# Kernel tuning notes

Measured on AMD Instinct MI355X. Metric: run time of the kernel, lower is better.

Reference implementation:

```python
import jax, jax.numpy as jnp
import numpy as np

N_NODES = 50000
N_EDGES = 800000
D = 128  # in_dim == hidden_dim


def setup_inputs() -> dict:
    key = jax.random.key(0)
    k1, k2, k3, k4 = jax.random.split(key, 4)
    x = jax.random.normal(k1, (N_NODES, D), dtype=jnp.float32)
    edge_index = jax.random.randint(k2, (2, N_EDGES), 0, N_NODES, dtype=jnp.int64)
    # Glorot-ish scale for square weights
    scale = 1.0 / np.sqrt(D)
    W1 = jax.random.normal(k3, (D, D), dtype=jnp.float32) * scale
    W2 = jax.random.normal(k4, (D, D), dtype=jnp.float32) * scale
    b1 = jnp.zeros((D,), dtype=jnp.float32)
    b2 = jnp.zeros((D,), dtype=jnp.float32)
    return {"x": x, "edge_index": edge_index, "W1": W1, "b1": b1, "W2": W2, "b2": b2}


def _gcn_layer(x, W, b, src, dst, norm, n):
    # PyG GCNConv: h = x @ W, then symmetric-normalized scatter-add, then + bias
    h = x @ W                                   # [N, D] dense GEMM
    msg = h[src] * norm[:, None]                # [E', D] gather + scale
    out = jax.ops.segment_sum(msg, dst, num_segments=n)  # scatter-add
    return out + b


def reference(x, edge_index, W1, b1, W2, b2):
    n = x.shape[0]
    # add self-loops (GCNConv default add_self_loops=True)
    loops = jnp.arange(n, dtype=edge_index.dtype)
    src = jnp.concatenate([edge_index[0], loops])
    dst = jnp.concatenate([edge_index[1], loops])
    # symmetric normalization: deg^{-1/2}[src] * deg^{-1/2}[dst]
    deg = jax.ops.segment_sum(jnp.ones_like(src, dtype=x.dtype), dst, num_segments=n)
    dinv = jax.lax.rsqrt(jnp.maximum(deg, 1.0))  # deg >= 1 due to self-loops
    norm = dinv[src] * dinv[dst]
    # layer 1: conv -> relu (dropout is identity in eval mode)
    h = jax.nn.relu(_gcn_layer(x, W1, b1, src, dst, norm, n))
    # layer 2 (cut='c2'): conv -> relu
    h = jax.nn.relu(_gcn_layer(h, W2, b2, src, dst, norm, n))
    return h
```

## Files before the change

### kernel.cpp

```cpp
#include <hip/hip_runtime.h>

#define NN 50000
#define NE 800000
#define DD 128
#define NSTRIP 3125
#define NB 196
#define CHUNK 4096
#define MAXB 6144

#define OF_LCNT  0
#define OF_LOFS  50176
#define OF_DINV  100352
#define OF_OFFS2 150528
#define OF_TMP2  250624
#define OF_CSRU  1053440
#define OF_H1    1655552
#define OF_H2    4855552
#define OF_W1H   8055552
#define OF_W1L   8063744
#define OF_W2H   8071936
#define OF_W2L   8080128

typedef __attribute__((ext_vector_type(8))) short bf8_t;
typedef __attribute__((ext_vector_type(8))) unsigned short us8;
typedef __attribute__((ext_vector_type(4))) float f32x4;

static __device__ __forceinline__ unsigned short f2bf(float f) {
    unsigned int u = __float_as_uint(f);
    unsigned int r = (u + 0x7fffu + ((u >> 16) & 1u)) >> 16;
    return (unsigned short)r;
}
static __device__ __forceinline__ float bf2f(unsigned short h) {
    return __uint_as_float(((unsigned int)h) << 16);
}

__global__ void k_wconv(const float* __restrict__ W1, const float* __restrict__ W2,
                        ushort* __restrict__ w1h, ushort* __restrict__ w1l,
                        ushort* __restrict__ w2h, ushort* __restrict__ w2l) {
    int gg = blockIdx.x * 256 + threadIdx.x;
    const float* W = (gg < 2048) ? W1 : W2;
    ushort* wh = (gg < 2048) ? w1h : w2h;
    ushort* wl = (gg < 2048) ? w1l : w2l;
    int g = gg & 2047;
    int ntile = g >> 8;
    int kk = (g >> 6) & 3;
    int lane = g & 63;
    int k0 = kk * 32 + ((lane >> 4) * 8);
    int col = ntile * 16 + (lane & 15);
#pragma unroll
    for (int j = 0; j < 8; ++j) {
        float w = W[(k0 + j) * DD + col];
        unsigned short h = f2bf(w);
        wh[(size_t)g * 8 + j] = h;
        wl[(size_t)g * 8 + j] = f2bf(w - bf2f(h));
    }
}

__global__ __launch_bounds__(256) void k_prep(
        const int* __restrict__ src, const int* __restrict__ dst,
        int* __restrict__ lcnt_g, int* __restrict__ lofs_g,
        unsigned int* __restrict__ tmp2,
        const float* __restrict__ X,
        const ushort* __restrict__ wh, const ushort* __restrict__ wl,
        ushort* __restrict__ H1) {
    __shared__ int lcnt[256];
    __shared__ int lsc[256];
    __shared__ int lcur[256];
    int tid = threadIdx.x;
    if (blockIdx.x < 196) {
        int blk = blockIdx.x;
        lcnt[tid] = 0;
        __syncthreads();
        int e0 = blk * CHUNK;
        int e1 = e0 + CHUNK; if (e1 > NE) e1 = NE;
        for (int e = e0 + tid; e < e1; e += 256)
            atomicAdd(&lcnt[dst[e] >> 8], 1);
        __syncthreads();
        int v = lcnt[tid];
        lsc[tid] = v;
        __syncthreads();
        for (int o = 1; o < 256; o <<= 1) {
            int t = (tid >= o) ? lsc[tid - o] : 0;
            __syncthreads();
            lsc[tid] += t;
            __syncthreads();
        }
        int excl = lsc[tid] - v;
        lcnt_g[tid * 196 + blk] = v;
        lofs_g[tid * 196 + blk] = excl;
        lcur[tid] = excl;
        __syncthreads();
        for (int e = e0 + tid; e < e1; e += 256) {
            int d = dst[e], s = src[e];
            int b = d >> 8;
            int r = atomicAdd(&lcur[b], 1);
            tmp2[blk * CHUNK + r] = ((unsigned int)s << 8) | (unsigned int)(d & 255);
        }
        return;
    }
    int wave = tid >> 6;
    int lane = tid & 63;
    int strip = (blockIdx.x - 196) * 4 + wave;
    if (strip >= NSTRIP) return;
    int rb = strip << 4;
    int m = lane & 15;
    int quad = lane >> 4;
    const float* ar = X + (size_t)(rb + m) * DD;
    f32x4 acc[8];
#pragma unroll
    for (int t = 0; t < 8; ++t) acc[t] = (f32x4){0.f, 0.f, 0.f, 0.f};
#pragma unroll
    for (int kk = 0; kk < 4; ++kk) {
        float4 xa = *(const float4*)(ar + kk * 32 + quad * 8);
        float4 xb = *(const float4*)(ar + kk * 32 + quad * 8 + 4);
        float xs[8] = {xa.x, xa.y, xa.z, xa.w, xb.x, xb.y, xb.z, xb.w};
        bf8_t ah, al;
#pragma unroll
        for (int j = 0; j < 8; ++j) {
            unsigned short hh = f2bf(xs[j]);
            ah[j] = (short)hh;
            al[j] = (short)f2bf(xs[j] - bf2f(hh));
        }
#pragma unroll
        for (int t = 0; t < 8; ++t) {
            size_t bo = ((size_t)(t * 4 + kk) * 64 + lane) * 8;
            bf8_t bh = *(const bf8_t*)(wh + bo);
            bf8_t bl = *(const bf8_t*)(wl + bo);
            acc[t] = __builtin_amdgcn_mfma_f32_16x16x32_bf16(ah, bh, acc[t], 0, 0, 0);
            acc[t] = __builtin_amdgcn_mfma_f32_16x16x32_bf16(ah, bl, acc[t], 0, 0, 0);
            acc[t] = __builtin_amdgcn_mfma_f32_16x16x32_bf16(al, bh, acc[t], 0, 0, 0);
        }
    }
#pragma unroll
    for (int t = 0; t < 8; ++t) {
#pragma unroll
        for (int r = 0; r < 4; ++r)
            H1[(size_t)(rb + quad * 4 + r) * DD + t * 16 + m] = f2bf(acc[t][r]);
    }
}

__global__ __launch_bounds__(256) void k_sort(const int* __restrict__ lcnt_g,
                                              const int* __restrict__ lofs_g,
                                              const unsigned int* __restrict__ tmp2,
                                              ushort* __restrict__ csru,
                                              int2* __restrict__ offs2,
                                              float* __restrict__ dinv) {
    __shared__ unsigned int ent[MAXB];
    __shared__ int c[256];
    __shared__ int p[256];
    __shared__ int o[256];
    __shared__ int cnt[256];
    __shared__ int boff[256];
    __shared__ int cur[256];
    int b = blockIdx.x, tid = threadIdx.x;
    int cv = (tid < 196) ? lcnt_g[b * 196 + tid] : 0;
    o[tid] = (tid < 196) ? lofs_g[b * 196 + tid] : 0;
    c[tid] = cv;
    p[tid] = cv;
    cnt[tid] = 0;
    __syncthreads();
    for (int s = 1; s < 256; s <<= 1) {
        int t = (tid >= s) ? p[tid - s] : 0;
        __syncthreads();
        p[tid] += t;
        __syncthreads();
    }
    int nb = p[255];
    for (int i = tid; i < nb; i += 256) {
        int lo = 0, hi = 255;
#pragma unroll
        for (int it = 0; it < 8; ++it) {
            int mid = (lo + hi) >> 1;
            if (p[mid] > i) hi = mid; else lo = mid + 1;
        }
        int blk = lo;
        int j = i - (p[blk] - c[blk]);
        unsigned int e = tmp2[blk * CHUNK + o[blk] + j];
        ent[i] = e;
        atomicAdd(&cnt[e & 255], 1);
    }
    __syncthreads();
    int v = cnt[tid];
    boff[tid] = v;
    __syncthreads();
    for (int s = 1; s < 256; s <<= 1) {
        int t = (tid >= s) ? boff[tid - s] : 0;
        __syncthreads();
        boff[tid] += t;
        __syncthreads();
    }
    int excl = boff[tid] - v;
    int base = b * MAXB;
    int node = b * 256 + tid;
    if (node < NN) {
        offs2[node] = make_int2(base + excl, base + excl + v);
        dinv[node] = rsqrtf((float)(v + 1));
    }
    cur[tid] = excl;
    __syncthreads();
    for (int i = tid; i < nb; i += 256) {
        unsigned int e = ent[i];
        int bin = e & 255;
        int r = atomicAdd(&cur[bin], 1);
        csru[base + r] = (ushort)(e >> 8);
    }
}

__global__ __launch_bounds__(512) void k_aggmm(const ushort* __restrict__ h1,
                                               const float* __restrict__ dinv,
                                               const int2* __restrict__ offs2,
                                               const ushort* __restrict__ csru,
                                               const float* __restrict__ b1,
                                               const ushort* __restrict__ w2h,
                                               const ushort* __restrict__ w2l,
                                               ushort* __restrict__ h2) {
    __shared__ float xs[16][136];
    int wave = threadIdx.x >> 6;
    int lane = threadIdx.x & 63;
    int rb = blockIdx.x * 16;
    int q = lane >> 4;
    int l = lane & 15;
    const float* bp = b1 + 8 * l;
    for (int nn = 0; nn < 2; ++nn) {
        int node = rb + wave * 2 + nn;
        float a0[8] = {0.f, 0.f, 0.f, 0.f, 0.f, 0.f, 0.f, 0.f};
        float a1[8] = {0.f, 0.f, 0.f, 0.f, 0.f, 0.f, 0.f, 0.f};
        float a2[8] = {0.f, 0.f, 0.f, 0.f, 0.f, 0.f, 0.f, 0.f};
        float a3[8] = {0.f, 0.f, 0.f, 0.f, 0.f, 0.f, 0.f, 0.f};
        int2 oe = offs2[node];
        int e  = oe.x + q;
        int e1 = oe.y;
        for (; e + 12 < e1; e += 16) {
            int s0 = csru[e];
            int s1 = csru[e + 4];
            int s2 = csru[e + 8];
            int s3 = csru[e + 12];
            float w0 = dinv[s0], w1 = dinv[s1], w2 = dinv[s2], w3 = dinv[s3];
            us8 v0 = *(const us8*)(h1 + (size_t)s0 * DD + 8 * l);
            us8 v1 = *(const us8*)(h1 + (size_t)s1 * DD + 8 * l);
            us8 v2 = *(const us8*)(h1 + (size_t)s2 * DD + 8 * l);
            us8 v3 = *(const us8*)(h1 + (size_t)s3 * DD + 8 * l);
#pragma unroll
            for (int j = 0; j < 8; ++j) {
                a0[j] += w0 * bf2f(v0[j]);
                a1[j] += w1 * bf2f(v1[j]);
                a2[j] += w2 * bf2f(v2[j]);
                a3[j] += w3 * bf2f(v3[j]);
            }
        }
        for (; e < e1; e += 4) {
            int s0 = csru[e];
            float w0 = dinv[s0];
            us8 v0 = *(const us8*)(h1 + (size_t)s0 * DD + 8 * l);
#pragma unroll
            for (int j = 0; j < 8; ++j) a0[j] += w0 * bf2f(v0[j]);
        }
        float dnode = dinv[node];
        if (q == 0) {
            us8 v = *(const us8*)(h1 + (size_t)node * DD + 8 * l);
#pragma unroll
            for (int j = 0; j < 8; ++j) a0[j] += dnode * bf2f(v[j]);
        }
#pragma unroll
        for (int j = 0; j < 8; ++j) {
            a0[j] += a1[j] + a2[j] + a3[j];
            a0[j] += __shfl_xor(a0[j], 16, 64);
            a0[j] += __shfl_xor(a0[j], 32, 64);
        }
        if (q == 0) {
            float* xr = &xs[wave * 2 + nn][8 * l];
#pragma unroll
            for (int j = 0; j < 8; ++j)
                xr[j] = fmaxf(dnode * a0[j] + bp[j], 0.f);
        }
    }
    __syncthreads();
    int m = lane & 15;
    int quad = lane >> 4;
    int t = wave;
    f32x4 acc = (f32x4){0.f, 0.f, 0.f, 0.f};
#pragma unroll
    for (int kk = 0; kk < 4; ++kk) {
        const float* xr = &xs[m][kk * 32 + quad * 8];
        float4 xa = *(const float4*)xr;
        float4 xb = *(const float4*)(xr + 4);
        float xv[8] = {xa.x, xa.y, xa.z, xa.w, xb.x, xb.y, xb.z, xb.w};
        bf8_t ah, al;
#pragma unroll
        for (int j = 0; j < 8; ++j) {
            unsigned short hh = f2bf(xv[j]);
            ah[j] = (short)hh;
            al[j] = (short)f2bf(xv[j] - bf2f(hh));
        }
        size_t bo = ((size_t)(t * 4 + kk) * 64 + lane) * 8;
        bf8_t bh = *(const bf8_t*)(w2h + bo);
        bf8_t bl = *(const bf8_t*)(w2l + bo);
        acc = __builtin_amdgcn_mfma_f32_16x16x32_bf16(ah, bh, acc, 0, 0, 0);
        acc = __builtin_amdgcn_mfma_f32_16x16x32_bf16(ah, bl, acc, 0, 0, 0);
        acc = __builtin_amdgcn_mfma_f32_16x16x32_bf16(al, bh, acc, 0, 0, 0);
    }
#pragma unroll
    for (int r = 0; r < 4; ++r)
        h2[(size_t)(rb + quad * 4 + r) * DD + t * 16 + m] = f2bf(acc[r]);
}

__global__ void k_agg(const ushort* __restrict__ h, const float* __restrict__ dinv,
                      const int2* __restrict__ offs2, const ushort* __restrict__ csru,
                      const float* __restrict__ bias, float* __restrict__ outf) {
    int wave = threadIdx.x >> 6;
    int lane = threadIdx.x & 63;
    int node = blockIdx.x * 4 + wave;
    int q = lane >> 4;
    int l = lane & 15;
    float a0[8] = {0.f, 0.f, 0.f, 0.f, 0.f, 0.f, 0.f, 0.f};
    float a1[8] = {0.f, 0.f, 0.f, 0.f, 0.f, 0.f, 0.f, 0.f};
    float a2[8] = {0.f, 0.f, 0.f, 0.f, 0.f, 0.f, 0.f, 0.f};
    float a3[8] = {0.f, 0.f, 0.f, 0.f, 0.f, 0.f, 0.f, 0.f};
    int2 oe = offs2[node];
    int e  = oe.x + q;
    int e1 = oe.y;
    for (; e + 12 < e1; e += 16) {
        int s0 = csru[e];
        int s1 = csru[e + 4];
        int s2 = csru[e + 8];
        int s3 = csru[e + 12];
        float w0 = dinv[s0], w1 = dinv[s1], w2 = dinv[s2], w3 = dinv[s3];
        us8 v0 = *(const us8*)(h + (size_t)s0 * DD + 8 * l);
        us8 v1 = *(const us8*)(h + (size_t)s1 * DD + 8 * l);
        us8 v2 = *(const us8*)(h + (size_t)s2 * DD + 8 * l);
        us8 v3 = *(const us8*)(h + (size_t)s3 * DD + 8 * l);
#pragma unroll
        for (int j = 0; j < 8; ++j) {
            a0[j] += w0 * bf2f(v0[j]);
            a1[j] += w1 * bf2f(v1[j]);
            a2[j] += w2 * bf2f(v2[j]);
            a3[j] += w3 * bf2f(v3[j]);
        }
    }
    for (; e < e1; e += 4) {
        int s0 = csru[e];
        float w0 = dinv[s0];
        us8 v0 = *(const us8*)(h + (size_t)s0 * DD + 8 * l);
#pragma unroll
        for (int j = 0; j < 8; ++j) a0[j] += w0 * bf2f(v0[j]);
    }
    float dnode = dinv[node];
    if (q == 0) {
        us8 v = *(const us8*)(h + (size_t)node * DD + 8 * l);
#pragma unroll
        for (int j = 0; j < 8; ++j) a0[j] += dnode * bf2f(v[j]);
    }
#pragma unroll
    for (int j = 0; j < 8; ++j) {
        a0[j] += a1[j] + a2[j] + a3[j];
        a0[j] += __shfl_xor(a0[j], 16, 64);
        a0[j] += __shfl_xor(a0[j], 32, 64);
    }
    if (q == 0) {
        float* op = outf + (size_t)node * DD + 8 * l;
        const float* bp = bias + 8 * l;
        float4 o0, o1;
        o0.x = fmaxf(dnode * a0[0] + bp[0], 0.f);
        o0.y = fmaxf(dnode * a0[1] + bp[1], 0.f);
        o0.z = fmaxf(dnode * a0[2] + bp[2], 0.f);
        o0.w = fmaxf(dnode * a0[3] + bp[3], 0.f);
        o1.x = fmaxf(dnode * a0[4] + bp[4], 0.f);
        o1.y = fmaxf(dnode * a0[5] + bp[5], 0.f);
        o1.z = fmaxf(dnode * a0[6] + bp[6], 0.f);
        o1.w = fmaxf(dnode * a0[7] + bp[7], 0.f);
        *(float4*)op = o0;
        *(float4*)(op + 4) = o1;
    }
}

extern "C" void kernel_launch(void* const* d_in, const int* in_sizes, int n_in,
                              void* d_out, int out_size, void* d_ws, size_t ws_size,
                              hipStream_t stream) {
    const float* x  = (const float*)d_in[0];
    const int*   ei = (const int*)d_in[1];
    const float* W1 = (const float*)d_in[2];
    const float* b1 = (const float*)d_in[3];
    const float* W2 = (const float*)d_in[4];
    const float* b2 = (const float*)d_in[5];
    float* out = (float*)d_out;

    const int* src = ei;
    const int* dst = ei + NE;

    int*          wsi  = (int*)d_ws;
    float*        wsf  = (float*)d_ws;
    ushort*       wsu  = (ushort*)d_ws;
    unsigned int* wsuw = (unsigned int*)d_ws;
    int*    lcnt_g = wsi + OF_LCNT;
    int*    lofs_g = wsi + OF_LOFS;
    float*  dinv   = wsf + OF_DINV;
    int2*   offs2  = (int2*)(wsi + OF_OFFS2);
    unsigned int* tmp2 = wsuw + OF_TMP2;
    ushort* csru   = wsu + (size_t)OF_CSRU * 2;
    ushort* h1     = wsu + (size_t)OF_H1 * 2;
    ushort* h2     = wsu + (size_t)OF_H2 * 2;
    ushort* w1h    = wsu + (size_t)OF_W1H * 2;
    ushort* w1l    = wsu + (size_t)OF_W1L * 2;
    ushort* w2h    = wsu + (size_t)OF_W2H * 2;
    ushort* w2l    = wsu + (size_t)OF_W2L * 2;

    hipLaunchKernelGGL(k_wconv, dim3(16), dim3(256), 0, stream,
                       W1, W2, w1h, w1l, w2h, w2l);
    hipLaunchKernelGGL(k_prep, dim3(196 + (NSTRIP + 3) / 4), dim3(256), 0, stream,
                       src, dst, lcnt_g, lofs_g, tmp2, x, w1h, w1l, h1);
    hipLaunchKernelGGL(k_sort, dim3(NB), dim3(256), 0, stream,
                       lcnt_g, lofs_g, tmp2, csru, offs2, dinv);
    hipLaunchKernelGGL(k_aggmm, dim3(NSTRIP), dim3(512), 0, stream,
                       h1, dinv, offs2, csru, b1, w2h, w2l, h2);
    hipLaunchKernelGGL(k_agg, dim3(NN / 4), dim3(256), 0, stream,
                       h2, dinv, offs2, csru, b2, out);
}
```

Before: 208.0 us.

## Prescale features by source dinv and split fused aggregate-GEMM into separate kernels

Source-side normalization is folded into the features ahead of time. k_sort writes g1 = dinv*h1, and the layer-2 GEMM writes g2 = dinv*(x@W2), so the aggregation loops drop the per-edge dinv gather and multiply. The fused k_aggmm kernel is replaced by a templated k_agg that writes hi/lo bf16 splits, followed by a standalone MFMA GEMM kernel. This removes random dinv loads per edge but adds a launch, extra hi/lo intermediate traffic through global memory, and an extra bf16 rounding of the prescaled features.

```diff
diff --git a/kernel.cpp b/kernel.cpp
--- a/kernel.cpp
+++ b/kernel.cpp
@@ -15,11 +15,14 @@
 #define OF_TMP2  250624
 #define OF_CSRU  1053440
 #define OF_H1    1655552
-#define OF_H2    4855552
-#define OF_W1H   8055552
-#define OF_W1L   8063744
-#define OF_W2H   8071936
-#define OF_W2L   8080128
+#define OF_G1    4855552
+#define OF_XH    8055552
+#define OF_XL    11255552
+#define OF_G2    14455552
+#define OF_W1H   17655552
+#define OF_W1L   17663744
+#define OF_W2H   17671936
+#define OF_W2L   17680128
 
 typedef __attribute__((ext_vector_type(8))) short bf8_t;
 typedef __attribute__((ext_vector_type(8))) unsigned short us8;
@@ -144,7 +147,9 @@
                                               const unsigned int* __restrict__ tmp2,
                                               ushort* __restrict__ csru,
                                               int2* __restrict__ offs2,
-                                              float* __restrict__ dinv) {
+                                              float* __restrict__ dinv,
+                                              const ushort* __restrict__ h1,
+                                              ushort* __restrict__ g1) {
     __shared__ unsigned int ent[MAXB];
     __shared__ int c[256];
     __shared__ int p[256];
@@ -152,6 +157,7 @@
     __shared__ int cnt[256];
     __shared__ int boff[256];
     __shared__ int cur[256];
+    __shared__ float sdinv[256];
     int b = blockIdx.x, tid = threadIdx.x;
     int cv = (tid < 196) ? lcnt_g[b * 196 + tid] : 0;
     o[tid] = (tid < 196) ? lofs_g[b * 196 + tid] : 0;
@@ -192,9 +198,11 @@
     int excl = boff[tid] - v;
     int base = b * MAXB;
     int node = b * 256 + tid;
+    float dv = rsqrtf((float)(v + 1));
+    sdinv[tid] = dv;
     if (node < NN) {
         offs2[node] = make_int2(base + excl, base + excl + v);
-        dinv[node] = rsqrtf((float)(v + 1));
+        dinv[node] = dv;
     }
     cur[tid] = excl;
     __syncthreads();
@@ -204,109 +212,26 @@
         int r = atomicAdd(&cur[bin], 1);
         csru[base + r] = (ushort)(e >> 8);
     }
-}
-
-__global__ __launch_bounds__(512) void k_aggmm(const ushort* __restrict__ h1,
-                                               const float* __restrict__ dinv,
-                                               const int2* __restrict__ offs2,
-                                               const ushort* __restrict__ csru,
-                                               const float* __restrict__ b1,
-                                               const ushort* __restrict__ w2h,
-                                               const ushort* __restrict__ w2l,
-                                               ushort* __restrict__ h2) {
-    __shared__ float xs[16][136];
-    int wave = threadIdx.x >> 6;
-    int lane = threadIdx.x & 63;
-    int rb = blockIdx.x * 16;
-    int q = lane >> 4;
-    int l = lane & 15;
-    const float* bp = b1 + 8 * l;
-    for (int nn = 0; nn < 2; ++nn) {
-        int node = rb + wave * 2 + nn;
-        float a0[8] = {0.f, 0.f, 0.f, 0.f, 0.f, 0.f, 0.f, 0.f};
-        float a1[8] = {0.f, 0.f, 0.f, 0.f, 0.f, 0.f, 0.f, 0.f};
-        float a2[8] = {0.f, 0.f, 0.f, 0.f, 0.f, 0.f, 0.f, 0.f};
-        float a3[8] = {0.f, 0.f, 0.f, 0.f, 0.f, 0.f, 0.f, 0.f};
-        int2 oe = offs2[node];
-        int e  = oe.x + q;
-        int e1 = oe.y;
-        for (; e + 12 < e1; e += 16) {
-            int s0 = csru[e];
-            int s1 = csru[e + 4];
-            int s2 = csru[e + 8];
-            int s3 = csru[e + 12];
-            float w0 = dinv[s0], w1 = dinv[s1], w2 = dinv[s2], w3 = dinv[s3];
-            us8 v0 = *(const us8*)(h1 + (size_t)s0 * DD + 8 * l);
-            us8 v1 = *(const us8*)(h1 + (size_t)s1 * DD + 8 * l);
-            us8 v2 = *(const us8*)(h1 + (size_t)s2 * DD + 8 * l);
-            us8 v3 = *(const us8*)(h1 + (size_t)s3 * DD + 8 * l);
-#pragma unroll
-            for (int j = 0; j < 8; ++j) {
-                a0[j] += w0 * bf2f(v0[j]);
-                a1[j] += w1 * bf2f(v1[j]);
-                a2[j] += w2 * bf2f(v2[j]);
-                a3[j] += w3 * bf2f(v3[j]);
-            }
-        }
-        for (; e < e1; e += 4) {
-            int s0 = csru[e];
-            float w0 = dinv[s0];
-            us8 v0 = *(const us8*)(h1 + (size_t)s0 * DD + 8 * l);
-#pragma unroll
-            for (int j = 0; j < 8; ++j) a0[j] += w0 * bf2f(v0[j]);
-        }
-        float dnode = dinv[node];
-        if (q == 0) {
-            us8 v = *(const us8*)(h1 + (size_t)node * DD + 8 * l);
-#pragma unroll
-            for (int j = 0; j < 8; ++j) a0[j] += dnode * bf2f(v[j]);
-        }
-#pragma unroll
-        for (int j = 0; j < 8; ++j) {
-            a0[j] += a1[j] + a2[j] + a3[j];
-            a0[j] += __shfl_xor(a0[j], 16, 64);
-            a0[j] += __shfl_xor(a0[j], 32, 64);
-        }
-        if (q == 0) {
-            float* xr = &xs[wave * 2 + nn][8 * l];
-#pragma unroll
-            for (int j = 0; j < 8; ++j)
-                xr[j] = fmaxf(dnode * a0[j] + bp[j], 0.f);
-        }
-    }
-    __syncthreads();
-    int m = lane & 15;
-    int quad = lane >> 4;
-    int t = wave;
-    f32x4 acc = (f32x4){0.f, 0.f, 0.f, 0.f};
-#pragma unroll
-    for (int kk = 0; kk < 4; ++kk) {
-        const float* xr = &xs[m][kk * 32 + quad * 8];
-        float4 xa = *(const float4*)xr;
-        float4 xb = *(const float4*)(xr + 4);
-        float xv[8] = {xa.x, xa.y, xa.z, xa.w, xb.x, xb.y, xb.z, xb.w};
-        bf8_t ah, al;
-#pragma unroll
-        for (int j = 0; j < 8; ++j) {
-            unsigned short hh = f2bf(xv[j]);
-            ah[j] = (short)hh;
-            al[j] = (short)f2bf(xv[j] - bf2f(hh));
-        }
-        size_t bo = ((size_t)(t * 4 + kk) * 64 + lane) * 8;
-        bf8_t bh = *(const bf8_t*)(w2h + bo);
-        bf8_t bl = *(const bf8_t*)(w2l + bo);
-        acc = __builtin_amdgcn_mfma_f32_16x16x32_bf16(ah, bh, acc, 0, 0, 0);
-        acc = __builtin_amdgcn_mfma_f32_16x16x32_bf16(ah, bl, acc, 0, 0, 0);
-        acc = __builtin_amdgcn_mfma_f32_16x16x32_bf16(al, bh, acc, 0, 0, 0);
-    }
-#pragma unroll
-    for (int r = 0; r < 4; ++r)
-        h2[(size_t)(rb + quad * 4 + r) * DD + t * 16 + m] = f2bf(acc[r]);
-}
-
-__global__ void k_agg(const ushort* __restrict__ h, const float* __restrict__ dinv,
+    int rmax = NN - b * 256;
+    if (rmax > 256) rmax = 256;
+    for (int ci = tid; ci < rmax * 16; ci += 256) {
+        int row = ci >> 4;
+        int c8 = ci & 15;
+        float dd = sdinv[row];
+        size_t idx = ((size_t)(b * 256 + row)) * DD + c8 * 8;
+        us8 hv = *(const us8*)(h1 + idx);
+        us8 gv;
+#pragma unroll
+        for (int j = 0; j < 8; ++j) gv[j] = f2bf(dd * bf2f(hv[j]));
+        *(us8*)(g1 + idx) = gv;
+    }
+}
+
+template <int OUTMODE>
+__global__ void k_agg(const ushort* __restrict__ g, const float* __restrict__ dinv,
                       const int2* __restrict__ offs2, const ushort* __restrict__ csru,
-                      const float* __restrict__ bias, float* __restrict__ outf) {
+                      const float* __restrict__ bias, float* __restrict__ outf,
+                      ushort* __restrict__ oh, ushort* __restrict__ ol) {
     int wave = threadIdx.x >> 6;
     int lane = threadIdx.x & 63;
     int node = blockIdx.x * 4 + wave;
@@ -324,31 +249,28 @@
         int s1 = csru[e + 4];
         int s2 = csru[e + 8];
         int s3 = csru[e + 12];
-        float w0 = dinv[s0], w1 = dinv[s1], w2 = dinv[s2], w3 = dinv[s3];
-        us8 v0 = *(const us8*)(h + (size_t)s0 * DD + 8 * l);
-        us8 v1 = *(const us8*)(h + (size_t)s1 * DD + 8 * l);
-        us8 v2 = *(const us8*)(h + (size_t)s2 * DD + 8 * l);
-        us8 v3 = *(const us8*)(h + (size_t)s3 * DD + 8 * l);
+        us8 v0 = *(const us8*)(g + (size_t)s0 * DD + 8 * l);
+        us8 v1 = *(const us8*)(g + (size_t)s1 * DD + 8 * l);
+        us8 v2 = *(const us8*)(g + (size_t)s2 * DD + 8 * l);
+        us8 v3 = *(const us8*)(g + (size_t)s3 * DD + 8 * l);
 #pragma unroll
         for (int j = 0; j < 8; ++j) {
-            a0[j] += w0 * bf2f(v0[j]);
-            a1[j] += w1 * bf2f(v1[j]);
-            a2[j] += w2 * bf2f(v2[j]);
-            a3[j] += w3 * bf2f(v3[j]);
+            a0[j] += bf2f(v0[j]);
+            a1[j] += bf2f(v1[j]);
+            a2[j] += bf2f(v2[j]);
+            a3[j] += bf2f(v3[j]);
         }
     }
     for (; e < e1; e += 4) {
         int s0 = csru[e];
-        float w0 = dinv[s0];
-        us8 v0 = *(const us8*)(h + (size_t)s0 * DD + 8 * l);
-#pragma unroll
-        for (int j = 0; j < 8; ++j) a0[j] += w0 * bf2f(v0[j]);
-    }
-    float dnode = dinv[node];
+        us8 v0 = *(const us8*)(g + (size_t)s0 * DD + 8 * l);
+#pragma unroll
+        for (int j = 0; j < 8; ++j) a0[j] += bf2f(v0[j]);
+    }
     if (q == 0) {
-        us8 v = *(const us8*)(h + (size_t)node * DD + 8 * l);
-#pragma unroll
-        for (int j = 0; j < 8; ++j) a0[j] += dnode * bf2f(v[j]);
+        us8 v = *(const us8*)(g + (size_t)node * DD + 8 * l);
+#pragma unroll
+        for (int j = 0; j < 8; ++j) a0[j] += bf2f(v[j]);
     }
 #pragma unroll
     for (int j = 0; j < 8; ++j) {
@@ -357,19 +279,71 @@
         a0[j] += __shfl_xor(a0[j], 32, 64);
     }
     if (q == 0) {
-        float* op = outf + (size_t)node * DD + 8 * l;
+        float dnode = dinv[node];
         const float* bp = bias + 8 * l;
-        float4 o0, o1;
-        o0.x = fmaxf(dnode * a0[0] + bp[0], 0.f);
-        o0.y = fmaxf(dnode * a0[1] + bp[1], 0.f);
-        o0.z = fmaxf(dnode * a0[2] + bp[2], 0.f);
-        o0.w = fmaxf(dnode * a0[3] + bp[3], 0.f);
-        o1.x = fmaxf(dnode * a0[4] + bp[4], 0.f);
-        o1.y = fmaxf(dnode * a0[5] + bp[5], 0.f);
-        o1.z = fmaxf(dnode * a0[6] + bp[6], 0.f);
-        o1.w = fmaxf(dnode * a0[7] + bp[7], 0.f);
-        *(float4*)op = o0;
-        *(float4*)(op + 4) = o1;
+        float r[8];
+#pragma unroll
+        for (int j = 0; j < 8; ++j) r[j] = fmaxf(dnode * a0[j] + bp[j], 0.f);
+        if (OUTMODE == 0) {
+            float* op = outf + (size_t)node * DD + 8 * l;
+            float4 o0 = {r[0], r[1], r[2], r[3]};
+            float4 o1 = {r[4], r[5], r[6], r[7]};
+            *(float4*)op = o0;
+            *(float4*)(op + 4) = o1;
+        } else {
+            us8 hh, ll;
+#pragma unroll
+            for (int j = 0; j < 8; ++j) {
+                unsigned short h = f2bf(r[j]);
+                hh[j] = h;
+                ll[j] = f2bf(r[j] - bf2f(h));
+            }
+            *(us8*)(oh + (size_t)node * DD + 8 * l) = hh;
+            *(us8*)(ol + (size_t)node * DD + 8 * l) = ll;
+        }
+    }
+}
+
+__global__ __launch_bounds__(256) void k_mgemm2(const ushort* __restrict__ xh,
+                                                const ushort* __restrict__ xl,
+                                                const ushort* __restrict__ wh,
+                                                const ushort* __restrict__ wl,
+                                                const float* __restrict__ dinv,
+                                                ushort* __restrict__ G) {
+    int wave = threadIdx.x >> 6;
+    int lane = threadIdx.x & 63;
+    int strip = blockIdx.x * 4 + wave;
+    if (strip >= NSTRIP) return;
+    int rb = strip << 4;
+    int m = lane & 15;
+    int quad = lane >> 4;
+    const ushort* arh = xh + (size_t)(rb + m) * DD;
+    const ushort* arl = xl + (size_t)(rb + m) * DD;
+    f32x4 acc[8];
+#pragma unroll
+    for (int t = 0; t < 8; ++t) acc[t] = (f32x4){0.f, 0.f, 0.f, 0.f};
+#pragma unroll
+    for (int kk = 0; kk < 4; ++kk) {
+        bf8_t ah = *(const bf8_t*)(arh + kk * 32 + quad * 8);
+        bf8_t al = *(const bf8_t*)(arl + kk * 32 + quad * 8);
+#pragma unroll
+        for (int t = 0; t < 8; ++t) {
+            size_t bo = ((size_t)(t * 4 + kk) * 64 + lane) * 8;
+            bf8_t bh = *(const bf8_t*)(wh + bo);
+            bf8_t bl = *(const bf8_t*)(wl + bo);
+            acc[t] = __builtin_amdgcn_mfma_f32_16x16x32_bf16(ah, bh, acc[t], 0, 0, 0);
+            acc[t] = __builtin_amdgcn_mfma_f32_16x16x32_bf16(ah, bl, acc[t], 0, 0, 0);
+            acc[t] = __builtin_amdgcn_mfma_f32_16x16x32_bf16(al, bh, acc[t], 0, 0, 0);
+        }
+    }
+    float dv[4];
+#pragma unroll
+    for (int r = 0; r < 4; ++r) dv[r] = dinv[rb + quad * 4 + r];
+#pragma unroll
+    for (int t = 0; t < 8; ++t) {
+#pragma unroll
+        for (int r = 0; r < 4; ++r)
+            G[(size_t)(rb + quad * 4 + r) * DD + t * 16 + m] = f2bf(dv[r] * acc[t][r]);
     }
 }
 
@@ -398,7 +372,10 @@
     unsigned int* tmp2 = wsuw + OF_TMP2;
     ushort* csru   = wsu + (size_t)OF_CSRU * 2;
     ushort* h1     = wsu + (size_t)OF_H1 * 2;
-    ushort* h2     = wsu + (size_t)OF_H2 * 2;
+    ushort* g1     = wsu + (size_t)OF_G1 * 2;
+    ushort* xh     = wsu + (size_t)OF_XH * 2;
+    ushort* xl     = wsu + (size_t)OF_XL * 2;
+    ushort* g2     = wsu + (size_t)OF_G2 * 2;
     ushort* w1h    = wsu + (size_t)OF_W1H * 2;
     ushort* w1l    = wsu + (size_t)OF_W1L * 2;
     ushort* w2h    = wsu + (size_t)OF_W2H * 2;
@@ -409,9 +386,11 @@
     hipLaunchKernelGGL(k_prep, dim3(196 + (NSTRIP + 3) / 4), dim3(256), 0, stream,
                        src, dst, lcnt_g, lofs_g, tmp2, x, w1h, w1l, h1);
     hipLaunchKernelGGL(k_sort, dim3(NB), dim3(256), 0, stream,
-                       lcnt_g, lofs_g, tmp2, csru, offs2, dinv);
-    hipLaunchKernelGGL(k_aggmm, dim3(NSTRIP), dim3(512), 0, stream,
-                       h1, dinv, offs2, csru, b1, w2h, w2l, h2);
-    hipLaunchKernelGGL(k_agg, dim3(NN / 4), dim3(256), 0, stream,
-                       h2, dinv, offs2, csru, b2, out);
-}
+                       lcnt_g, lofs_g, tmp2, csru, offs2, dinv, h1, g1);
+    hipLaunchKernelGGL(k_agg<1>, dim3(NN / 4), dim3(256), 0, stream,
+                       g1, dinv, offs2, csru, b1, (float*)nullptr, xh, xl);
+    hipLaunchKernelGGL(k_mgemm2, dim3((NSTRIP + 3) / 4), dim3(256), 0, stream,
+                       xh, xl, w2h, w2l, dinv, g2);
+    hipLaunchKernelGGL(k_agg<0>, dim3(NN / 4), dim3(256), 0, stream,
+                       g2, dinv, offs2, csru, b2, out, (ushort*)nullptr, (ushort*)nullptr);
+}
```

Measured after the change: 222.0 us. +6.7%, slower.

## Prescale features by source dinv to remove per-edge dinv gathers

Applied to the files above, without the earlier changes.

Folds the source-side dinv factor into the node features before aggregation. k_sort writes a scaled copy g1 = dinv*h1, and k_aggmm writes g2 already scaled by dinv. The aggregation loops then sum raw rows without gathering dinv[src] per edge and without a multiply per element. In exchange, k_sort gains an extra full read and write pass over h1, and the pre-scaled values are rounded to bf16 a second time, which slightly changes numerics.

```diff
diff --git a/kernel.cpp b/kernel.cpp
--- a/kernel.cpp
+++ b/kernel.cpp
@@ -15,11 +15,12 @@
 #define OF_TMP2  250624
 #define OF_CSRU  1053440
 #define OF_H1    1655552
-#define OF_H2    4855552
-#define OF_W1H   8055552
-#define OF_W1L   8063744
-#define OF_W2H   8071936
-#define OF_W2L   8080128
+#define OF_G1    4855552
+#define OF_G2    8055552
+#define OF_W1H   11255552
+#define OF_W1L   11263744
+#define OF_W2H   11271936
+#define OF_W2L   11280128
 
 typedef __attribute__((ext_vector_type(8))) short bf8_t;
 typedef __attribute__((ext_vector_type(8))) unsigned short us8;
@@ -144,7 +145,9 @@
                                               const unsigned int* __restrict__ tmp2,
                                               ushort* __restrict__ csru,
                                               int2* __restrict__ offs2,
-                                              float* __restrict__ dinv) {
+                                              float* __restrict__ dinv,
+                                              const ushort* __restrict__ h1,
+                                              ushort* __restrict__ g1) {
     __shared__ unsigned int ent[MAXB];
     __shared__ int c[256];
     __shared__ int p[256];
@@ -152,6 +155,7 @@
     __shared__ int cnt[256];
     __shared__ int boff[256];
     __shared__ int cur[256];
+    __shared__ float sdinv[256];
     int b = blockIdx.x, tid = threadIdx.x;
     int cv = (tid < 196) ? lcnt_g[b * 196 + tid] : 0;
     o[tid] = (tid < 196) ? lofs_g[b * 196 + tid] : 0;
@@ -192,9 +196,11 @@
     int excl = boff[tid] - v;
     int base = b * MAXB;
     int node = b * 256 + tid;
+    float dv = rsqrtf((float)(v + 1));
+    sdinv[tid] = dv;
     if (node < NN) {
         offs2[node] = make_int2(base + excl, base + excl + v);
-        dinv[node] = rsqrtf((float)(v + 1));
+        dinv[node] = dv;
     }
     cur[tid] = excl;
     __syncthreads();
@@ -204,17 +210,30 @@
         int r = atomicAdd(&cur[bin], 1);
         csru[base + r] = (ushort)(e >> 8);
     }
-}
-
-__global__ __launch_bounds__(512) void k_aggmm(const ushort* __restrict__ h1,
+    int rmax = NN - b * 256;
+    if (rmax > 256) rmax = 256;
+    for (int ci = tid; ci < rmax * 16; ci += 256) {
+        int row = ci >> 4;
+        int c8 = ci & 15;
+        float dd = sdinv[row];
+        size_t idx = ((size_t)(b * 256 + row)) * DD + c8 * 8;
+        us8 hv = *(const us8*)(h1 + idx);
+        us8 gv;
+#pragma unroll
+        for (int j = 0; j < 8; ++j) gv[j] = f2bf(dd * bf2f(hv[j]));
+        *(us8*)(g1 + idx) = gv;
+    }
+}
+
+__global__ __launch_bounds__(512) void k_aggmm(const ushort* __restrict__ g1,
                                                const float* __restrict__ dinv,
                                                const int2* __restrict__ offs2,
                                                const ushort* __restrict__ csru,
                                                const float* __restrict__ b1,
                                                const ushort* __restrict__ w2h,
                                                const ushort* __restrict__ w2l,
-                                               ushort* __restrict__ h2) {
-    __shared__ float xs[16][136];
+                                               ushort* __restrict__ g2) {
+    __shared__ float xs[16][132];
     int wave = threadIdx.x >> 6;
     int lane = threadIdx.x & 63;
     int rb = blockIdx.x * 16;
@@ -235,31 +254,28 @@
             int s1 = csru[e + 4];
             int s2 = csru[e + 8];
             int s3 = csru[e + 12];
-            float w0 = dinv[s0], w1 = dinv[s1], w2 = dinv[s2], w3 = dinv[s3];
-            us8 v0 = *(const us8*)(h1 + (size_t)s0 * DD + 8 * l);
-            us8 v1 = *(const us8*)(h1 + (size_t)s1 * DD + 8 * l);
-            us8 v2 = *(const us8*)(h1 + (size_t)s2 * DD + 8 * l);
-            us8 v3 = *(const us8*)(h1 + (size_t)s3 * DD + 8 * l);
+            us8 v0 = *(const us8*)(g1 + (size_t)s0 * DD + 8 * l);
+            us8 v1 = *(const us8*)(g1 + (size_t)s1 * DD + 8 * l);
+            us8 v2 = *(const us8*)(g1 + (size_t)s2 * DD + 8 * l);
+            us8 v3 = *(const us8*)(g1 + (size_t)s3 * DD + 8 * l);
 #pragma unroll
             for (int j = 0; j < 8; ++j) {
-                a0[j] += w0 * bf2f(v0[j]);
-                a1[j] += w1 * bf2f(v1[j]);
-                a2[j] += w2 * bf2f(v2[j]);
-                a3[j] += w3 * bf2f(v3[j]);
+                a0[j] += bf2f(v0[j]);
+                a1[j] += bf2f(v1[j]);
+                a2[j] += bf2f(v2[j]);
+                a3[j] += bf2f(v3[j]);
             }
         }
         for (; e < e1; e += 4) {
             int s0 = csru[e];
-            float w0 = dinv[s0];
-            us8 v0 = *(const us8*)(h1 + (size_t)s0 * DD + 8 * l);
-#pragma unroll
-            for (int j = 0; j < 8; ++j) a0[j] += w0 * bf2f(v0[j]);
-        }
-        float dnode = dinv[node];
+            us8 v0 = *(const us8*)(g1 + (size_t)s0 * DD + 8 * l);
+#pragma unroll
+            for (int j = 0; j < 8; ++j) a0[j] += bf2f(v0[j]);
+        }
         if (q == 0) {
-            us8 v = *(const us8*)(h1 + (size_t)node * DD + 8 * l);
-#pragma unroll
-            for (int j = 0; j < 8; ++j) a0[j] += dnode * bf2f(v[j]);
+            us8 v = *(const us8*)(g1 + (size_t)node * DD + 8 * l);
+#pragma unroll
+            for (int j = 0; j < 8; ++j) a0[j] += bf2f(v[j]);
         }
 #pragma unroll
         for (int j = 0; j < 8; ++j) {
@@ -268,6 +284,7 @@
             a0[j] += __shfl_xor(a0[j], 32, 64);
         }
         if (q == 0) {
+            float dnode = dinv[node];
             float* xr = &xs[wave * 2 + nn][8 * l];
 #pragma unroll
             for (int j = 0; j < 8; ++j)
@@ -299,12 +316,15 @@
         acc = __builtin_amdgcn_mfma_f32_16x16x32_bf16(ah, bl, acc, 0, 0, 0);
         acc = __builtin_amdgcn_mfma_f32_16x16x32_bf16(al, bh, acc, 0, 0, 0);
     }
+    float dv[4];
+#pragma unroll
+    for (int r = 0; r < 4; ++r) dv[r] = dinv[rb + quad * 4 + r];
 #pragma unroll
     for (int r = 0; r < 4; ++r)
-        h2[(size_t)(rb + quad * 4 + r) * DD + t * 16 + m] = f2bf(acc[r]);
-}
-
-__global__ void k_agg(const ushort* __restrict__ h, const float* __restrict__ dinv,
+        g2[(size_t)(rb + quad * 4 + r) * DD + t * 16 + m] = f2bf(dv[r] * acc[r]);
+}
+
+__global__ void k_agg(const ushort* __restrict__ g, const float* __restrict__ dinv,
                       const int2* __restrict__ offs2, const ushort* __restrict__ csru,
                       const float* __restrict__ bias, float* __restrict__ outf) {
     int wave = threadIdx.x >> 6;
@@ -324,31 +344,28 @@
         int s1 = csru[e + 4];
         int s2 = csru[e + 8];
         int s3 = csru[e + 12];
-        float w0 = dinv[s0], w1 = dinv[s1], w2 = dinv[s2], w3 = dinv[s3];
-        us8 v0 = *(const us8*)(h + (size_t)s0 * DD + 8 * l);
-        us8 v1 = *(const us8*)(h + (size_t)s1 * DD + 8 * l);
-        us8 v2 = *(const us8*)(h + (size_t)s2 * DD + 8 * l);
-        us8 v3 = *(const us8*)(h + (size_t)s3 * DD + 8 * l);
+        us8 v0 = *(const us8*)(g + (size_t)s0 * DD + 8 * l);
+        us8 v1 = *(const us8*)(g + (size_t)s1 * DD + 8 * l);
+        us8 v2 = *(const us8*)(g + (size_t)s2 * DD + 8 * l);
+        us8 v3 = *(const us8*)(g + (size_t)s3 * DD + 8 * l);
 #pragma unroll
         for (int j = 0; j < 8; ++j) {
-            a0[j] += w0 * bf2f(v0[j]);
-            a1[j] += w1 * bf2f(v1[j]);
-            a2[j] += w2 * bf2f(v2[j]);
-            a3[j] += w3 * bf2f(v3[j]);
+            a0[j] += bf2f(v0[j]);
+            a1[j] += bf2f(v1[j]);
+            a2[j] += bf2f(v2[j]);
+            a3[j] += bf2f(v3[j]);
         }
     }
     for (; e < e1; e += 4) {
         int s0 = csru[e];
-        float w0 = dinv[s0];
-        us8 v0 = *(const us8*)(h + (size_t)s0 * DD + 8 * l);
-#pragma unroll
-        for (int j = 0; j < 8; ++j) a0[j] += w0 * bf2f(v0[j]);
-    }
-    float dnode = dinv[node];
+        us8 v0 = *(const us8*)(g + (size_t)s0 * DD + 8 * l);
+#pragma unroll
+        for (int j = 0; j < 8; ++j) a0[j] += bf2f(v0[j]);
+    }
     if (q == 0) {
-        us8 v = *(const us8*)(h + (size_t)node * DD + 8 * l);
-#pragma unroll
-        for (int j = 0; j < 8; ++j) a0[j] += dnode * bf2f(v[j]);
+        us8 v = *(const us8*)(g + (size_t)node * DD + 8 * l);
+#pragma unroll
+        for (int j = 0; j < 8; ++j) a0[j] += bf2f(v[j]);
     }
 #pragma unroll
     for (int j = 0; j < 8; ++j) {
@@ -357,6 +374,7 @@
         a0[j] += __shfl_xor(a0[j], 32, 64);
     }
     if (q == 0) {
+        float dnode = dinv[node];
         float* op = outf + (size_t)node * DD + 8 * l;
         const float* bp = bias + 8 * l;
         float4 o0, o1;
@@ -398,7 +416,8 @@
     unsigned int* tmp2 = wsuw + OF_TMP2;
     ushort* csru   = wsu + (size_t)OF_CSRU * 2;
     ushort* h1     = wsu + (size_t)OF_H1 * 2;
-    ushort* h2     = wsu + (size_t)OF_H2 * 2;
+    ushort* g1     = wsu + (size_t)OF_G1 * 2;
+    ushort* g2     = wsu + (size_t)OF_G2 * 2;
     ushort* w1h    = wsu + (size_t)OF_W1H * 2;
     ushort* w1l    = wsu + (size_t)OF_W1L * 2;
     ushort* w2h    = wsu + (size_t)OF_W2H * 2;
@@ -409,9 +428,9 @@
     hipLaunchKernelGGL(k_prep, dim3(196 + (NSTRIP + 3) / 4), dim3(256), 0, stream,
                        src, dst, lcnt_g, lofs_g, tmp2, x, w1h, w1l, h1);
     hipLaunchKernelGGL(k_sort, dim3(NB), dim3(256), 0, stream,
-                       lcnt_g, lofs_g, tmp2, csru, offs2, dinv);
+                       lcnt_g, lofs_g, tmp2, csru, offs2, dinv, h1, g1);
     hipLaunchKernelGGL(k_aggmm, dim3(NSTRIP), dim3(512), 0, stream,
-                       h1, dinv, offs2, csru, b1, w2h, w2l, h2);
+                       g1, dinv, offs2, csru, b1, w2h, w2l, g2);
     hipLaunchKernelGGL(k_agg, dim3(NN / 4), dim3(256), 0, stream,
-                       h2, dinv, offs2, csru, b2, out);
-}
+                       g2, dinv, offs2, csru, b2, out);
+}
```

After: 226.2 us. 8.7% more time.
